# Kernel optimization log

Hardware: AMD Instinct MI355X
Metric: run time of the kernel (lower is better)

## Reference

```python
import jax, jax.numpy as jnp
import numpy as np

T_CH = 512
C_CH = 512
RED = 16
K = int(T_CH * 0.3)  # 153


def setup_inputs() -> dict:
    key = jax.random.key(0)
    ks = jax.random.split(key, 12)
    h_t, h_c = T_CH // RED, C_CH // RED
    s = 0.05
    return {
        "x_t": jax.random.normal(ks[0], (16, T_CH, 64, 64), jnp.float32),
        "x_c": jax.random.normal(ks[1], (16, C_CH, 64, 64), jnp.float32),
        # SE branch t: Linear(T,T/r) -> ReLU -> Linear(T/r,T) -> Sigmoid (weights stored as (in,out))
        "w1_t": jax.random.normal(ks[2], (T_CH, h_t), jnp.float32) * s,
        "b1_t": jnp.zeros((h_t,), jnp.float32),
        "w2_t": jax.random.normal(ks[3], (h_t, T_CH), jnp.float32) * s,
        "b2_t": jnp.zeros((T_CH,), jnp.float32),
        # SE branch c
        "w1_c": jax.random.normal(ks[4], (C_CH, h_c), jnp.float32) * s,
        "b1_c": jnp.zeros((h_c,), jnp.float32),
        "w2_c": jax.random.normal(ks[5], (h_c, C_CH), jnp.float32) * s,
        "b2_c": jnp.zeros((C_CH,), jnp.float32),
        # cross-channel attention parameter, shape (t_channels, c_channels)
        "cross_att": jax.random.normal(ks[6], (T_CH, C_CH), jnp.float32),
    }


def reference(x_t, x_c, w1_t, b1_t, w2_t, b2_t, w1_c, b1_c, w2_c, b2_c, cross_att):
    ct = x_t.shape[1]
    # AdaptiveAvgPool2d(1) -> global mean over spatial, then SE MLP + sigmoid
    att_t = jnp.mean(x_t, axis=(2, 3))                      # [b, ct]
    att_t = jax.nn.sigmoid(jax.nn.relu(att_t @ w1_t + b1_t) @ w2_t + b2_t)
    att_c = jnp.mean(x_c, axis=(2, 3))                      # [b, cc]
    att_c = jax.nn.sigmoid(jax.nn.relu(att_c @ w1_c + b1_c) @ w2_c + b2_c)

    # top-k hard mask over t-channels (scatter of constant 1.0)
    _, topk_idx = jax.lax.top_k(att_t, K)                   # [b, K]
    sparse_att_t = jax.nn.one_hot(topk_idx, ct, dtype=att_t.dtype).sum(axis=1)  # [b, ct]

    cross_w = jax.nn.softmax(cross_att, axis=-1)            # [ct, cc]

    # einsum('bt,tc,bchw->bthw'): GEMM over channels then broadcast mask
    cross_t = sparse_att_t[:, :, None, None] * jnp.einsum('tc,bchw->bthw', cross_w, x_c)
    # einsum('bc,tc,bthw->bchw') with cross_w.T labeled 'tc' => sum_t cross_w[c,t] * x_t
    cross_c = att_c[:, :, None, None] * jnp.einsum('ct,bthw->bchw', cross_w, x_t)

    out_t = x_t * att_t[:, :, None, None] + cross_t
    out_c = x_c * att_c[:, :, None, None] + cross_c
    return out_t, out_c
```

## Files before the change

kernel.cpp:

```cpp
#include <hip/hip_runtime.h>

#define NBATCH 16
#define CH 512
#define HID 32
#define KTOP 153
#define SP 4096
#define NELEM (NBATCH*CH*SP)

typedef __bf16 bf16x8 __attribute__((ext_vector_type(8)));
typedef float f32x16 __attribute__((ext_vector_type(16)));

__device__ __forceinline__ unsigned short f2bf(float f) {
    union { float f; unsigned u; } v; v.f = f;
    unsigned r = v.u + 0x7FFFu + ((v.u >> 16) & 1u);
    return (unsigned short)(r >> 16);
}

__device__ __forceinline__ void gld_lds16(const void* g, void* l) {
    __builtin_amdgcn_global_load_lds(
        (__attribute__((address_space(1))) unsigned int*)g,
        (__attribute__((address_space(3))) unsigned int*)l, 16, 0, 0);
}

__global__ __launch_bounds__(256) void k1_reduce_transpose(
    const float* __restrict__ xt, const float* __restrict__ xc,
    unsigned short* __restrict__ xbt, unsigned short* __restrict__ xbc,
    float* __restrict__ psum)
{
    int sb = blockIdx.x, chb = blockIdx.y, bz = blockIdx.z;
    int b = bz >> 1, br = bz & 1;
    const float* x = br ? xc : xt;
    unsigned short* xb = br ? xbc : xbt;
    int t = threadIdx.x, lane = t & 63, w = t >> 6;
    int s0 = sb * 64, ch0 = chb * 64;

    __shared__ unsigned short T[64 * 68];

    float vals[16];
    const float* xbase = x + (size_t)b * CH * SP + s0 + lane;
    #pragma unroll
    for (int it = 0; it < 4; ++it)
        #pragma unroll
        for (int i = 0; i < 4; ++i) {
            int chl = w * 4 + i + 16 * it;
            vals[it * 4 + i] = xbase[(size_t)(ch0 + chl) * SP];
        }

    #pragma unroll
    for (int it = 0; it < 4; ++it) {
        int chl = w * 4 + 16 * it;
        ushort4 p;
        p.x = f2bf(vals[it * 4 + 0]); p.y = f2bf(vals[it * 4 + 1]);
        p.z = f2bf(vals[it * 4 + 2]); p.w = f2bf(vals[it * 4 + 3]);
        *(ushort4*)&T[lane * 68 + chl] = p;
    }

    #pragma unroll
    for (int k = 0; k < 16; ++k) {
        float v = vals[k];
        #pragma unroll
        for (int off = 32; off; off >>= 1) v += __shfl_xor(v, off, 64);
        vals[k] = v;
    }
    if (lane < 16) {
        int it = lane >> 2, i = lane & 3;
        int chl = w * 4 + i + 16 * it;
        psum[(((size_t)(br * 16 + b)) * CH + ch0 + chl) * 64 + sb] = vals[lane];
    }

    __syncthreads();
    size_t orow = (size_t)b * SP + s0;
    #pragma unroll
    for (int q = 0; q < 4; ++q) {
        int gid = q * 256 + t;
        int sl = gid >> 4;
        int c4 = (gid & 15) * 4;
        ushort4 d = *(const ushort4*)&T[sl * 68 + c4];
        *(ushort4*)&xb[(orow + sl) * CH + ch0 + c4] = d;
    }
}

__global__ __launch_bounds__(512) void k2_se(
    const float* __restrict__ psum,
    const float* __restrict__ w1t, const float* __restrict__ b1t,
    const float* __restrict__ w2t, const float* __restrict__ b2t,
    const float* __restrict__ w1c, const float* __restrict__ b1c,
    const float* __restrict__ w2c, const float* __restrict__ b2c,
    float* __restrict__ sAt, float* __restrict__ sBt, float* __restrict__ attc)
{
    int b = blockIdx.x, br = blockIdx.y;
    int t = threadIdx.x;
    __shared__ float satt[512];
    __shared__ float sh[32];
    __shared__ float sval[512];

    const float* pr = psum + (((size_t)(br * 16 + b)) * CH + t) * 64;
    float s = 0.f;
    #pragma unroll
    for (int j = 0; j < 64; ++j) s += pr[j];
    satt[t] = s * (1.0f / 4096.0f);
    __syncthreads();

    const float* w1 = br ? w1c : w1t; const float* b1 = br ? b1c : b1t;
    const float* w2 = br ? w2c : w2t; const float* b2 = br ? b2c : b2t;

    if (t < HID) {
        float h = b1[t];
        for (int i = 0; i < CH; ++i) h += satt[i] * w1[i * HID + t];
        sh[t] = fmaxf(h, 0.0f);
    }
    __syncthreads();
    float z = b2[t];
    #pragma unroll
    for (int j = 0; j < HID; ++j) z += sh[j] * w2[j * CH + t];
    float a = 1.0f / (1.0f + expf(-z));

    if (br == 0) {
        sval[t] = a;
        __syncthreads();
        int cnt = 0;
        for (int j = 0; j < CH; ++j) {
            float o = sval[j];
            cnt += (o > a) || (o == a && j < t);
        }
        sAt[b * CH + t] = a;
        sBt[b * CH + t] = (cnt < KTOP) ? 1.0f : 0.0f;
    } else {
        attc[b * CH + t] = a;
    }
}

__global__ __launch_bounds__(64) void k2_softmax(
    const float* __restrict__ ca, unsigned short* __restrict__ wswz)
{
    int trow = blockIdx.x;
    int lane = threadIdx.x;
    const float* row = ca + (size_t)trow * CH;
    float v[8];
    #pragma unroll
    for (int i = 0; i < 8; ++i) v[i] = row[lane * 8 + i];
    float m = v[0];
    #pragma unroll
    for (int i = 1; i < 8; ++i) m = fmaxf(m, v[i]);
    #pragma unroll
    for (int off = 32; off; off >>= 1) m = fmaxf(m, __shfl_xor(m, off, 64));
    float s = 0.f;
    #pragma unroll
    for (int i = 0; i < 8; ++i) { v[i] = expf(v[i] - m); s += v[i]; }
    #pragma unroll
    for (int off = 32; off; off >>= 1) s += __shfl_xor(s, off, 64);
    float inv = 1.0f / s;

    int k = lane * 8;
    int kb = k >> 5, ks = (k >> 4) & 1, hi = (k >> 3) & 1;
    int p = ((kb * 16 + (trow >> 5)) * 2 + ks) * 64 + hi * 32 + (trow & 31);
    unsigned short* dst = wswz + (size_t)p * 8;
    ushort4 lo, hm;
    lo.x = f2bf(v[0] * inv); lo.y = f2bf(v[1] * inv);
    lo.z = f2bf(v[2] * inv); lo.w = f2bf(v[3] * inv);
    hm.x = f2bf(v[4] * inv); hm.y = f2bf(v[5] * inv);
    hm.z = f2bf(v[6] * inv); hm.w = f2bf(v[7] * inv);
    *(ushort4*)dst = lo;
    *(ushort4*)(dst + 4) = hm;
}

__global__ __launch_bounds__(256) void k3_gemm(
    const unsigned short* __restrict__ xbt, const unsigned short* __restrict__ xbc,
    const unsigned short* __restrict__ wswz,
    const float* __restrict__ xt, const float* __restrict__ xc,
    const float* __restrict__ sAt, const float* __restrict__ sBt,
    const float* __restrict__ attc,
    float* __restrict__ out)
{
    int nt = blockIdx.x, b = blockIdx.y, g = blockIdx.z;
    int t = threadIdx.x, lane = t & 63, w = t >> 6;
    int n0 = nt * 64;

    const unsigned short* xb = g ? xbt : xbc;
    const float* xref = g ? xc : xt;
    const float* sA = g ? attc : sAt;
    const float* sB = g ? attc : sBt;

    __shared__ __align__(16) unsigned short As[16384];
    __shared__ __align__(16) unsigned short Bs[2048];

    f32x16 acc[4][2];
    #pragma unroll
    for (int r = 0; r < 4; ++r)
        #pragma unroll
        for (int c = 0; c < 2; ++c)
            #pragma unroll
            for (int e = 0; e < 16; ++e) acc[r][c][e] = 0.0f;

    int bks = t >> 7, bcn = (t >> 6) & 1;
    const unsigned short* bgp = xb
        + ((size_t)b * SP + n0 + bcn * 32 + (lane & 31)) * CH
        + bks * 16 + (lane >> 5) * 8;
    unsigned short* bl = &Bs[t * 8];

    for (int kb = 0; kb < 16; ++kb) {
        __syncthreads();
        const unsigned short* ag = wswz + kb * 16384;
        #pragma unroll
        for (int i = 0; i < 8; ++i) {
            int gid = i * 256 + t;
            gld_lds16(ag + gid * 8, &As[gid * 8]);
        }
        gld_lds16(bgp + kb * 32, bl);
        __syncthreads();

        #pragma unroll
        for (int ks = 0; ks < 2; ++ks) {
            bf16x8 af[4], bfr[2];
            #pragma unroll
            for (int r = 0; r < 4; ++r)
                af[r] = *(const bf16x8*)&As[(((w * 4 + r) * 2 + ks) * 64 + lane) * 8];
            #pragma unroll
            for (int c = 0; c < 2; ++c)
                bfr[c] = *(const bf16x8*)&Bs[((ks * 2 + c) * 64 + lane) * 8];
            #pragma unroll
            for (int r = 0; r < 4; ++r)
                #pragma unroll
                for (int c = 0; c < 2; ++c)
                    acc[r][c] = __builtin_amdgcn_mfma_f32_32x32x16_bf16(
                        af[r], bfr[c], acc[r][c], 0, 0, 0);
        }
    }

    size_t outg = (size_t)g * NELEM;
    int colbase = n0 + (lane & 31);
    int rowq = 4 * (lane >> 5);
    #pragma unroll
    for (int r = 0; r < 4; ++r) {
        #pragma unroll
        for (int c = 0; c < 2; ++c) {
            int col = colbase + c * 32;
            #pragma unroll
            for (int reg = 0; reg < 16; ++reg) {
                int m = w * 128 + r * 32 + (reg & 3) + 8 * (reg >> 2) + rowq;
                size_t idx = ((size_t)b * CH + m) * SP + col;
                float xv = xref[idx];
                float sav = sA[b * CH + m];
                float sbv = sB[b * CH + m];
                out[outg + idx] = sav * xv + sbv * acc[r][c][reg];
            }
        }
    }
}

extern "C" void kernel_launch(void* const* d_in, const int* in_sizes, int n_in,
                              void* d_out, int out_size, void* d_ws, size_t ws_size,
                              hipStream_t stream)
{
    const float* xt  = (const float*)d_in[0];
    const float* xc  = (const float*)d_in[1];
    const float* w1t = (const float*)d_in[2];
    const float* b1t = (const float*)d_in[3];
    const float* w2t = (const float*)d_in[4];
    const float* b2t = (const float*)d_in[5];
    const float* w1c = (const float*)d_in[6];
    const float* b1c = (const float*)d_in[7];
    const float* w2c = (const float*)d_in[8];
    const float* b2c = (const float*)d_in[9];
    const float* ca  = (const float*)d_in[10];
    float* out = (float*)d_out;
    char* ws = (char*)d_ws;

    unsigned short* xbt  = (unsigned short*)(ws);
    unsigned short* xbc  = (unsigned short*)(ws + 67108864ull);
    unsigned short* wswz = (unsigned short*)(ws + 134217728ull);
    float* psum = (float*)(ws + 134742016ull);
    float* sAt  = (float*)(ws + 138936320ull);
    float* sBt  = (float*)(ws + 138969088ull);
    float* attc = (float*)(ws + 139001856ull);

    hipLaunchKernelGGL(k1_reduce_transpose, dim3(64, 8, 32), dim3(256), 0, stream,
                       xt, xc, xbt, xbc, psum);
    hipLaunchKernelGGL(k2_se, dim3(16, 2), dim3(512), 0, stream,
                       psum, w1t, b1t, w2t, b2t, w1c, b1c, w2c, b2c, sAt, sBt, attc);
    hipLaunchKernelGGL(k2_softmax, dim3(512), dim3(64), 0, stream, ca, wswz);
    hipLaunchKernelGGL(k3_gemm, dim3(64, 16, 2), dim3(256), 0, stream,
                       xbt, xbc, wswz, xt, xc, sAt, sBt, attc, out);
}
```

Baseline: 716.3 us.

## Load GEMM operands directly to registers with double buffering, restructure reduce layout

The GEMM kernel no longer stages A and B tiles through LDS with two barriers per k-step. Each wave now loads its fragments straight from global memory into double-buffered registers, prefetching the next k-block while issuing MFMAs on the current one, and a two-blocks-per-SM launch bound is added. The reduce/transpose kernel stages fp32 tiles in padded LDS, computing row sums there instead of with shuffles, and writes partial sums in a layout that gives coalesced reads in the SE kernel. The SE kernel also parallelises the first MLP layer across all threads. Loading fragments directly from global gives up LDS reuse and relies on cache hits across waves, and the register double buffer adds register pressure.

```diff
diff --git a/kernel.cpp b/kernel.cpp
--- a/kernel.cpp
+++ b/kernel.cpp
@@ -16,12 +16,6 @@
     return (unsigned short)(r >> 16);
 }
 
-__device__ __forceinline__ void gld_lds16(const void* g, void* l) {
-    __builtin_amdgcn_global_load_lds(
-        (__attribute__((address_space(1))) unsigned int*)g,
-        (__attribute__((address_space(3))) unsigned int*)l, 16, 0, 0);
-}
-
 __global__ __launch_bounds__(256) void k1_reduce_transpose(
     const float* __restrict__ xt, const float* __restrict__ xc,
     unsigned short* __restrict__ xbt, unsigned short* __restrict__ xbc,
@@ -34,48 +28,45 @@
     int t = threadIdx.x, lane = t & 63, w = t >> 6;
     int s0 = sb * 64, ch0 = chb * 64;
 
-    __shared__ unsigned short T[64 * 68];
-
-    float vals[16];
+    __shared__ float G[64 * 73];
+
     const float* xbase = x + (size_t)b * CH * SP + s0 + lane;
     #pragma unroll
     for (int it = 0; it < 4; ++it)
         #pragma unroll
         for (int i = 0; i < 4; ++i) {
             int chl = w * 4 + i + 16 * it;
-            vals[it * 4 + i] = xbase[(size_t)(ch0 + chl) * SP];
-        }
-
-    #pragma unroll
-    for (int it = 0; it < 4; ++it) {
-        int chl = w * 4 + 16 * it;
-        ushort4 p;
-        p.x = f2bf(vals[it * 4 + 0]); p.y = f2bf(vals[it * 4 + 1]);
-        p.z = f2bf(vals[it * 4 + 2]); p.w = f2bf(vals[it * 4 + 3]);
-        *(ushort4*)&T[lane * 68 + chl] = p;
-    }
-
-    #pragma unroll
-    for (int k = 0; k < 16; ++k) {
-        float v = vals[k];
-        #pragma unroll
-        for (int off = 32; off; off >>= 1) v += __shfl_xor(v, off, 64);
-        vals[k] = v;
-    }
-    if (lane < 16) {
-        int it = lane >> 2, i = lane & 3;
-        int chl = w * 4 + i + 16 * it;
-        psum[(((size_t)(br * 16 + b)) * CH + ch0 + chl) * 64 + sb] = vals[lane];
-    }
-
-    __syncthreads();
+            G[chl * 73 + lane] = xbase[(size_t)(ch0 + chl) * SP];
+        }
+    __syncthreads();
+
+    {
+        int chl = t & 63, q = t >> 6;
+        const float* row = &G[chl * 73 + q * 16];
+        float s = 0.f;
+        #pragma unroll
+        for (int i = 0; i < 16; ++i) s += row[i];
+        G[chl * 73 + 64 + q] = s;
+    }
+    __syncthreads();
+
+    if (t < 64) {
+        const float* p = &G[t * 73 + 64];
+        float s = p[0] + p[1] + p[2] + p[3];
+        psum[((size_t)sb * 32 + (br * 16 + b)) * CH + ch0 + t] = s;
+    }
+
     size_t orow = (size_t)b * SP + s0;
     #pragma unroll
     for (int q = 0; q < 4; ++q) {
         int gid = q * 256 + t;
         int sl = gid >> 4;
         int c4 = (gid & 15) * 4;
-        ushort4 d = *(const ushort4*)&T[sl * 68 + c4];
+        ushort4 d;
+        d.x = f2bf(G[(c4 + 0) * 73 + sl]);
+        d.y = f2bf(G[(c4 + 1) * 73 + sl]);
+        d.z = f2bf(G[(c4 + 2) * 73 + sl]);
+        d.w = f2bf(G[(c4 + 3) * 73 + sl]);
         *(ushort4*)&xb[(orow + sl) * CH + ch0 + c4] = d;
     }
 }
@@ -89,27 +80,39 @@
     float* __restrict__ sAt, float* __restrict__ sBt, float* __restrict__ attc)
 {
     int b = blockIdx.x, br = blockIdx.y;
+    int bb = br * 16 + b;
     int t = threadIdx.x;
     __shared__ float satt[512];
+    __shared__ float ph[16][33];
     __shared__ float sh[32];
     __shared__ float sval[512];
 
-    const float* pr = psum + (((size_t)(br * 16 + b)) * CH + t) * 64;
     float s = 0.f;
     #pragma unroll
-    for (int j = 0; j < 64; ++j) s += pr[j];
+    for (int j = 0; j < 64; ++j) s += psum[((size_t)j * 32 + bb) * CH + t];
     satt[t] = s * (1.0f / 4096.0f);
     __syncthreads();
 
     const float* w1 = br ? w1c : w1t; const float* b1 = br ? b1c : b1t;
     const float* w2 = br ? w2c : w2t; const float* b2 = br ? b2c : b2t;
 
+    {
+        int j = t & 31, seg = t >> 5;
+        float hp = 0.f;
+        #pragma unroll
+        for (int i = 0; i < 32; ++i)
+            hp += satt[seg * 32 + i] * w1[(seg * 32 + i) * HID + j];
+        ph[seg][j] = hp;
+    }
+    __syncthreads();
     if (t < HID) {
         float h = b1[t];
-        for (int i = 0; i < CH; ++i) h += satt[i] * w1[i * HID + t];
+        #pragma unroll
+        for (int sgi = 0; sgi < 16; ++sgi) h += ph[sgi][t];
         sh[t] = fmaxf(h, 0.0f);
     }
     __syncthreads();
+
     float z = b2[t];
     #pragma unroll
     for (int j = 0; j < HID; ++j) z += sh[j] * w2[j * CH + t];
@@ -164,7 +167,7 @@
     *(ushort4*)(dst + 4) = hm;
 }
 
-__global__ __launch_bounds__(256) void k3_gemm(
+__global__ __launch_bounds__(256, 2) void k3_gemm(
     const unsigned short* __restrict__ xbt, const unsigned short* __restrict__ xbc,
     const unsigned short* __restrict__ wswz,
     const float* __restrict__ xt, const float* __restrict__ xc,
@@ -181,9 +184,6 @@
     const float* sA = g ? attc : sAt;
     const float* sB = g ? attc : sBt;
 
-    __shared__ __align__(16) unsigned short As[16384];
-    __shared__ __align__(16) unsigned short Bs[2048];
-
     f32x16 acc[4][2];
     #pragma unroll
     for (int r = 0; r < 4; ++r)
@@ -192,39 +192,48 @@
             #pragma unroll
             for (int e = 0; e < 16; ++e) acc[r][c][e] = 0.0f;
 
-    int bks = t >> 7, bcn = (t >> 6) & 1;
-    const unsigned short* bgp = xb
-        + ((size_t)b * SP + n0 + bcn * 32 + (lane & 31)) * CH
-        + bks * 16 + (lane >> 5) * 8;
-    unsigned short* bl = &Bs[t * 8];
-
+    const unsigned short* abase = wswz + ((size_t)(w * 4 * 2 * 64 + lane)) * 8;
+    const unsigned short* bbase = xb + ((size_t)b * SP + n0 + (lane & 31)) * CH
+                                     + (lane >> 5) * 8;
+
+    bf16x8 afr[2][8], bfr[2][4];
+
+    #pragma unroll
+    for (int r = 0; r < 4; ++r)
+        #pragma unroll
+        for (int ks = 0; ks < 2; ++ks)
+            afr[0][r * 2 + ks] = *(const bf16x8*)(abase + r * 1024 + ks * 512);
+    #pragma unroll
+    for (int c = 0; c < 2; ++c)
+        #pragma unroll
+        for (int ks = 0; ks < 2; ++ks)
+            bfr[0][c * 2 + ks] = *(const bf16x8*)(bbase + c * 16384 + ks * 16);
+
+    #pragma unroll
     for (int kb = 0; kb < 16; ++kb) {
-        __syncthreads();
-        const unsigned short* ag = wswz + kb * 16384;
-        #pragma unroll
-        for (int i = 0; i < 8; ++i) {
-            int gid = i * 256 + t;
-            gld_lds16(ag + gid * 8, &As[gid * 8]);
-        }
-        gld_lds16(bgp + kb * 32, bl);
-        __syncthreads();
-
-        #pragma unroll
-        for (int ks = 0; ks < 2; ++ks) {
-            bf16x8 af[4], bfr[2];
+        int cur = kb & 1, nxt = cur ^ 1;
+        if (kb < 15) {
             #pragma unroll
             for (int r = 0; r < 4; ++r)
-                af[r] = *(const bf16x8*)&As[(((w * 4 + r) * 2 + ks) * 64 + lane) * 8];
+                #pragma unroll
+                for (int ks = 0; ks < 2; ++ks)
+                    afr[nxt][r * 2 + ks] =
+                        *(const bf16x8*)(abase + (kb + 1) * 16384 + r * 1024 + ks * 512);
             #pragma unroll
             for (int c = 0; c < 2; ++c)
-                bfr[c] = *(const bf16x8*)&Bs[((ks * 2 + c) * 64 + lane) * 8];
+                #pragma unroll
+                for (int ks = 0; ks < 2; ++ks)
+                    bfr[nxt][c * 2 + ks] =
+                        *(const bf16x8*)(bbase + c * 16384 + (kb + 1) * 32 + ks * 16);
+        }
+        #pragma unroll
+        for (int ks = 0; ks < 2; ++ks)
             #pragma unroll
             for (int r = 0; r < 4; ++r)
                 #pragma unroll
                 for (int c = 0; c < 2; ++c)
                     acc[r][c] = __builtin_amdgcn_mfma_f32_32x32x16_bf16(
-                        af[r], bfr[c], acc[r][c], 0, 0, 0);
-        }
+                        afr[cur][r * 2 + ks], bfr[cur][c * 2 + ks], acc[r][c], 0, 0, 0);
     }
 
     size_t outg = (size_t)g * NELEM;
@@ -233,16 +242,14 @@
     #pragma unroll
     for (int r = 0; r < 4; ++r) {
         #pragma unroll
-        for (int c = 0; c < 2; ++c) {
-            int col = colbase + c * 32;
-            #pragma unroll
-            for (int reg = 0; reg < 16; ++reg) {
-                int m = w * 128 + r * 32 + (reg & 3) + 8 * (reg >> 2) + rowq;
-                size_t idx = ((size_t)b * CH + m) * SP + col;
-                float xv = xref[idx];
-                float sav = sA[b * CH + m];
-                float sbv = sB[b * CH + m];
-                out[outg + idx] = sav * xv + sbv * acc[r][c][reg];
+        for (int reg = 0; reg < 16; ++reg) {
+            int m = w * 128 + r * 32 + (reg & 3) + 8 * (reg >> 2) + rowq;
+            float sav = sA[b * CH + m];
+            float sbv = sB[b * CH + m];
+            #pragma unroll
+            for (int c = 0; c < 2; ++c) {
+                size_t idx = ((size_t)b * CH + m) * SP + colbase + c * 32;
+                out[outg + idx] = sav * xref[idx] + sbv * acc[r][c][reg];
             }
         }
     }
```

New measurement: 712.9 us. Within noise of the previous version (-0.5%).
